# Kernel optimization log

Measured on AMD Instinct MI355X. Metric: run time of the kernel, lower is better.

The kernel has to match this reference:

```python
import jax, jax.numpy as jnp
import numpy as np
from math import pi as PI, log

B, N, D, K = 16, 16384, 64, 64


def setup_inputs() -> dict:
    key = jax.random.key(0)
    k1, k2, k3, k4 = jax.random.split(key, 4)
    x = jax.random.normal(k1, (B, N, D), dtype=jnp.float32)
    pi_w = jax.nn.softmax(jax.random.normal(k2, (K,), dtype=jnp.float32))  # mixture weights, sum to 1
    mu = jax.random.normal(k3, (K, D), dtype=jnp.float32)
    var = jax.random.uniform(k4, (K, D), dtype=jnp.float32, minval=0.5, maxval=1.5)  # diagonal variances
    return {"x": x, "pi": pi_w, "mu": mu, "var": var}


def reference(x, pi, mu, var):
    b, n, d = x.shape
    # --- gmm.predict_proba: diagonal-covariance Gaussian log-likelihoods + log pi, softmax over K ---
    inv_var = 1.0 / var                                   # (K, D)
    x2 = x * x                                            # (B, N, D)
    # Mahalanobis distance expanded via matmuls to avoid a (B,N,K,D) intermediate
    maha = (jnp.einsum('bnd,kd->bnk', x2, inv_var)
            - 2.0 * jnp.einsum('bnd,kd->bnk', x, mu * inv_var)
            + jnp.sum(mu * mu * inv_var, axis=-1))        # (B, N, K)
    log_det = jnp.sum(jnp.log(var), axis=-1)              # (K,)
    log_prob = -0.5 * (d * log(2.0 * PI) + log_det + maha)
    Q = jax.nn.softmax(log_prob + jnp.log(pi), axis=-1)   # (B, N, K) responsibilities
    # --- weighted reductions over N ---
    Q_sum = jnp.sum(Q, axis=1) / n                         # (B, K)
    Q_x = jnp.einsum('bnk,bnd->bkd', Q, x) / n             # (B, K, D)
    Q_x2 = jnp.einsum('bnk,bnd->bkd', Q, x2) / n           # (B, K, D)
    # --- Fisher-vector statistics ---
    d_pi = Q_sum - pi                                      # (B, K)
    qs = Q_sum[..., None]                                  # (B, K, 1)
    d_mu = Q_x - qs * mu
    d_sigma = -Q_x2 - qs * (mu * mu) + qs * var + 2.0 * Q_x * mu
    return jnp.concatenate([d_pi.reshape(b, -1), d_mu.reshape(b, -1), d_sigma.reshape(b, -1)], axis=1)
```

## Files before the change

kernel.cpp:

```cpp
#include <hip/hip_runtime.h>
#include <hip/hip_bf16.h>
#include <math.h>

#define B_  16
#define N_  16384
#define D_  64
#define K_  64
#define OUT_PER_B (K_ + 2*K_*D_)
#define CHUNKS 32
#define NTILES (N_ / CHUNKS / 64)

#define PART_STRIDE (64*4 + 2*4096*2)

typedef float f32x4 __attribute__((ext_vector_type(4)));
typedef short short8 __attribute__((ext_vector_type(8)));

union U8 { short8 s8; unsigned int u[4]; };

__device__ __forceinline__ unsigned short f2bf(float f) {
    union { float f; unsigned int u; } v; v.f = f;
    unsigned int r = v.u + 0x7FFFu + ((v.u >> 16) & 1u);
    return (unsigned short)(r >> 16);
}

__device__ __forceinline__ unsigned int f2bf2(float lo, float hi) {
    __hip_bfloat162 h = __float22bfloat162_rn(make_float2(lo, hi));
    unsigned int u;
    __builtin_memcpy(&u, &h, 4);
    return u;
}

__device__ __forceinline__ float bf2f(unsigned short u) {
    unsigned int v = ((unsigned int)u) << 16;
    float f;
    __builtin_memcpy(&f, &v, 4);
    return f;
}

__global__ __launch_bounds__(256, 2) void fv_main(const float* __restrict__ x,
                                                  const float* __restrict__ pi,
                                                  const float* __restrict__ mu,
                                                  const float* __restrict__ var,
                                                  char* __restrict__ partials) {
    __shared__ __align__(16) unsigned short QtS[2][64 * 72];
    __shared__ float qsum_s[4][64];
    __shared__ float red[256];
    __shared__ float c0s[64];

    const int t    = threadIdx.x;
    const int w    = t >> 6;
    const int lane = t & 63;
    const int r16  = lane & 15;
    const int q    = lane >> 4;

    {
        int k = t >> 2, pr = t & 3;
        float s = 0.0f;
        #pragma unroll
        for (int j = 0; j < 16; ++j) {
            int d = pr * 16 + j;
            float v = var[k * 64 + d];
            float m = mu[k * 64 + d];
            s += __logf(v) + m * m / v;
        }
        red[t] = s;
    }

    short8 wfrag[4][4];
    #pragma unroll
    for (int kt = 0; kt < 4; ++kt) {
        const int k = 16 * kt + r16;
        const float* vr = var + k * 64 + 8 * q;
        const float* mr = mu  + k * 64 + 8 * q;
        float vv[16], mm[16];
        *(float4*)&vv[0]  = *(const float4*)(vr);
        *(float4*)&vv[4]  = *(const float4*)(vr + 4);
        *(float4*)&vv[8]  = *(const float4*)(vr + 32);
        *(float4*)&vv[12] = *(const float4*)(vr + 36);
        *(float4*)&mm[0]  = *(const float4*)(mr);
        *(float4*)&mm[4]  = *(const float4*)(mr + 4);
        *(float4*)&mm[8]  = *(const float4*)(mr + 32);
        *(float4*)&mm[12] = *(const float4*)(mr + 36);
        float iv[16];
        #pragma unroll
        for (int i = 0; i < 16; ++i) iv[i] = 1.0f / vv[i];
        U8 h0, h1, h2, h3;
        #pragma unroll
        for (int i = 0; i < 4; ++i) {
            h0.u[i] = f2bf2(-0.5f * iv[2*i],     -0.5f * iv[2*i + 1]);
            h1.u[i] = f2bf2(-0.5f * iv[8 + 2*i], -0.5f * iv[8 + 2*i + 1]);
            h2.u[i] = f2bf2(mm[2*i] * iv[2*i],   mm[2*i+1] * iv[2*i + 1]);
            h3.u[i] = f2bf2(mm[8+2*i] * iv[8+2*i], mm[8+2*i+1] * iv[8+2*i+1]);
        }
        wfrag[kt][0] = h0.s8; wfrag[kt][1] = h1.s8;
        wfrag[kt][2] = h2.s8; wfrag[kt][3] = h3.s8;
    }

    __syncthreads();
    if ((t & 3) == 0) {
        int k = t >> 2;
        float sum = red[4 * k] + red[4 * k + 1] + red[4 * k + 2] + red[4 * k + 3];
        c0s[k] = __logf(pi[k]) - 0.5f * (117.6241322502f + sum);
    }
    __syncthreads();

    f32x4 c0v[4];
    #pragma unroll
    for (int kt = 0; kt < 4; ++kt)
        c0v[kt] = *(const f32x4*)&c0s[16 * kt + 4 * q];

    const int bi    = blockIdx.y;
    const int chunk = blockIdx.x;
    const int ppb   = N_ / CHUNKS;
    const float* xb = x + ((size_t)bi * N_ + (size_t)chunk * ppb) * D_;

    f32x4 accX[4]  = {};
    f32x4 accX2[4] = {};
    float qsacc[4][4] = {};

    const int rowoff = (16 * w + r16) * D_ + 8 * q;
    const int dcol   = 16 * w + r16;

    float4 va, vb, vc, vd;
    {
        const float* xr = xb + rowoff;
        va = *(const float4*)(xr);
        vb = *(const float4*)(xr + 4);
        vc = *(const float4*)(xr + 32);
        vd = *(const float4*)(xr + 36);
    }

    #pragma unroll 2
    for (int tile = 0; tile < NTILES; ++tile) {
        const float* xt = xb + (size_t)tile * 64 * D_;

        float vle[16];
        {
            const float* xc = xt + dcol;
            #pragma unroll
            for (int c = 0; c < 2; ++c)
                #pragma unroll
                for (int j = 0; j < 8; ++j)
                    vle[8 * c + j] = xc[(32 * c + 8 * q + j) * D_];
        }

        float4 nva, nvb, nvc, nvd;
        if (tile + 1 < NTILES) {
            const float* xr = xt + 64 * D_ + rowoff;
            nva = *(const float4*)(xr);
            nvb = *(const float4*)(xr + 4);
            nvc = *(const float4*)(xr + 32);
            nvd = *(const float4*)(xr + 36);
        }

        U8 fxa, fxb, fx2a, fx2b;
        fxa.u[0]  = f2bf2(va.x, va.y);           fxa.u[1]  = f2bf2(va.z, va.w);
        fxa.u[2]  = f2bf2(vb.x, vb.y);           fxa.u[3]  = f2bf2(vb.z, vb.w);
        fxb.u[0]  = f2bf2(vc.x, vc.y);           fxb.u[1]  = f2bf2(vc.z, vc.w);
        fxb.u[2]  = f2bf2(vd.x, vd.y);           fxb.u[3]  = f2bf2(vd.z, vd.w);
        fx2a.u[0] = f2bf2(va.x*va.x, va.y*va.y); fx2a.u[1] = f2bf2(va.z*va.z, va.w*va.w);
        fx2a.u[2] = f2bf2(vb.x*vb.x, vb.y*vb.y); fx2a.u[3] = f2bf2(vb.z*vb.z, vb.w*vb.w);
        fx2b.u[0] = f2bf2(vc.x*vc.x, vc.y*vc.y); fx2b.u[1] = f2bf2(vc.z*vc.z, vc.w*vc.w);
        fx2b.u[2] = f2bf2(vd.x*vd.x, vd.y*vd.y); fx2b.u[3] = f2bf2(vd.z*vd.z, vd.w*vd.w);

        float sc[4][4];
        #pragma unroll
        for (int kt = 0; kt < 4; ++kt) {
            f32x4 a = c0v[kt];
            a = __builtin_amdgcn_mfma_f32_16x16x32_bf16(wfrag[kt][0], fx2a.s8, a, 0, 0, 0);
            a = __builtin_amdgcn_mfma_f32_16x16x32_bf16(wfrag[kt][1], fx2b.s8, a, 0, 0, 0);
            a = __builtin_amdgcn_mfma_f32_16x16x32_bf16(wfrag[kt][2], fxa.s8,  a, 0, 0, 0);
            a = __builtin_amdgcn_mfma_f32_16x16x32_bf16(wfrag[kt][3], fxb.s8,  a, 0, 0, 0);
            sc[kt][0] = a[0]; sc[kt][1] = a[1]; sc[kt][2] = a[2]; sc[kt][3] = a[3];
        }

        float mx = sc[0][0];
        #pragma unroll
        for (int kt = 0; kt < 4; ++kt)
            #pragma unroll
            for (int rr = 0; rr < 4; ++rr) mx = fmaxf(mx, sc[kt][rr]);
        mx = fmaxf(mx, __shfl_xor(mx, 16));
        mx = fmaxf(mx, __shfl_xor(mx, 32));
        float z = 0.0f;
        #pragma unroll
        for (int kt = 0; kt < 4; ++kt)
            #pragma unroll
            for (int rr = 0; rr < 4; ++rr) {
                sc[kt][rr] = __expf(sc[kt][rr] - mx);
                z += sc[kt][rr];
            }
        z += __shfl_xor(z, 16);
        z += __shfl_xor(z, 32);
        float inv = 1.0f / z;
        const int p = 16 * w + r16;
        unsigned short* Qb = QtS[tile & 1];
        #pragma unroll
        for (int kt = 0; kt < 4; ++kt) {
            #pragma unroll
            for (int rr = 0; rr < 4; rr += 2) {
                float q0 = sc[kt][rr] * inv;
                float q1 = sc[kt][rr + 1] * inv;
                qsacc[kt][rr]     += q0;
                qsacc[kt][rr + 1] += q1;
                unsigned int pk = f2bf2(q0, q1);
                Qb[(16 * kt + 4 * q + rr)     * 72 + p] = (unsigned short)pk;
                Qb[(16 * kt + 4 * q + rr + 1) * 72 + p] = (unsigned short)(pk >> 16);
            }
        }

        asm volatile("s_waitcnt lgkmcnt(0)\n\ts_barrier" ::: "memory");

        U8 fxp0, fxp1, fx2p0, fx2p1;
        #pragma unroll
        for (int i = 0; i < 4; ++i) {
            float a0 = vle[2 * i], a1 = vle[2 * i + 1];
            float b0 = vle[8 + 2 * i], b1 = vle[8 + 2 * i + 1];
            fxp0.u[i]  = f2bf2(a0, a1);
            fxp1.u[i]  = f2bf2(b0, b1);
            fx2p0.u[i] = f2bf2(a0 * a0, a1 * a1);
            fx2p1.u[i] = f2bf2(b0 * b0, b1 * b1);
        }
        #pragma unroll
        for (int kt = 0; kt < 4; ++kt) {
            const unsigned short* qr = &Qb[(16 * kt + r16) * 72 + 8 * q];
            short8 aq0 = *(const short8*)(const void*)(qr);
            short8 aq1 = *(const short8*)(const void*)(qr + 32);
            accX[kt]  = __builtin_amdgcn_mfma_f32_16x16x32_bf16(aq0, fxp0.s8,  accX[kt],  0, 0, 0);
            accX2[kt] = __builtin_amdgcn_mfma_f32_16x16x32_bf16(aq0, fx2p0.s8, accX2[kt], 0, 0, 0);
            accX[kt]  = __builtin_amdgcn_mfma_f32_16x16x32_bf16(aq1, fxp1.s8,  accX[kt],  0, 0, 0);
            accX2[kt] = __builtin_amdgcn_mfma_f32_16x16x32_bf16(aq1, fx2p1.s8, accX2[kt], 0, 0, 0);
        }

        va = nva; vb = nvb; vc = nvc; vd = nvd;
    }

    char* rec = partials + ((size_t)bi * CHUNKS + chunk) * PART_STRIDE;
    float* part_qs = (float*)rec;
    unsigned short* part_qx  = (unsigned short*)(rec + 256);
    unsigned short* part_qx2 = part_qx + 4096;
    #pragma unroll
    for (int kt = 0; kt < 4; ++kt)
        #pragma unroll
        for (int rr = 0; rr < 4; ++rr) {
            int k = 16 * kt + 4 * q + rr;
            part_qx [k * 64 + 16 * w + r16] = f2bf(accX[kt][rr]);
            part_qx2[k * 64 + 16 * w + r16] = f2bf(accX2[kt][rr]);
        }
    #pragma unroll
    for (int kt = 0; kt < 4; ++kt)
        #pragma unroll
        for (int rr = 0; rr < 4; ++rr) {
            float v = qsacc[kt][rr];
            v += __shfl_xor(v, 1);
            v += __shfl_xor(v, 2);
            v += __shfl_xor(v, 4);
            v += __shfl_xor(v, 8);
            if (r16 == 0) qsum_s[w][16 * kt + 4 * q + rr] = v;
        }
    __syncthreads();
    if (t < 64)
        part_qs[t] = qsum_s[0][t] + qsum_s[1][t] + qsum_s[2][t] + qsum_s[3][t];
}

__global__ __launch_bounds__(256) void fv_finalize(const float* __restrict__ pi,
                                                   const float* __restrict__ mu,
                                                   const float* __restrict__ var,
                                                   const char* __restrict__ partials,
                                                   float* __restrict__ out) {
    int g = blockIdx.x * 256 + threadIdx.x;
    if (g >= B_ * OUT_PER_B) return;
    int b   = g / OUT_PER_B;
    int pos = g - b * OUT_PER_B;
    const char* base = partials + (size_t)b * CHUNKS * PART_STRIDE;
    const float invN = 1.0f / (float)N_;

    if (pos < 64) {
        float qs = 0.0f;
        for (int c = 0; c < CHUNKS; ++c)
            qs += ((const float*)(base + c * PART_STRIDE))[pos];
        out[g] = qs * invN - pi[pos];
    } else if (pos < 64 + 4096) {
        int idx = pos - 64;
        int k = idx >> 6;
        float qs = 0.0f, qx = 0.0f;
        for (int c = 0; c < CHUNKS; ++c) {
            const char* r = base + c * PART_STRIDE;
            qs += ((const float*)r)[k];
            qx += bf2f(((const unsigned short*)(r + 256))[idx]);
        }
        out[g] = (qx - qs * mu[idx]) * invN;
    } else {
        int idx = pos - 64 - 4096;
        int k = idx >> 6;
        float qs = 0.0f, qx = 0.0f, qx2 = 0.0f;
        for (int c = 0; c < CHUNKS; ++c) {
            const char* r = base + c * PART_STRIDE;
            qs  += ((const float*)r)[k];
            qx  += bf2f(((const unsigned short*)(r + 256))[idx]);
            qx2 += bf2f(((const unsigned short*)(r + 256))[4096 + idx]);
        }
        float m = mu[idx], v = var[idx];
        out[g] = (-qx2 - qs * m * m + qs * v + 2.0f * qx * m) * invN;
    }
}

extern "C" void kernel_launch(void* const* d_in, const int* in_sizes, int n_in,
                              void* d_out, int out_size, void* d_ws, size_t ws_size,
                              hipStream_t stream) {
    const float* x   = (const float*)d_in[0];
    const float* pi  = (const float*)d_in[1];
    const float* mu  = (const float*)d_in[2];
    const float* var = (const float*)d_in[3];
    char* partials = (char*)d_ws;

    fv_main<<<dim3(CHUNKS, B_), 256, 0, stream>>>(x, pi, mu, var, partials);
    int total = B_ * OUT_PER_B;
    fv_finalize<<<(total + 255) / 256, 256, 0, stream>>>(pi, mu, var, partials,
                                                         (float*)d_out);
}
```

Measured before the change: 120.1 us.

## Double chunk count, raise occupancy, restructure finalize per (batch, component)

Doubles the number of N-chunks per batch so the main kernel launches 1024 blocks instead of 512, and raises the launch-bounds min-blocks hint from 2 to 4 to allow more resident waves. The finalize kernel is rewritten so each block handles one (b,k) pair. Four thread groups split the chunk reduction and combine through shared memory, and Q_sum, Q_x and Q_x2 are computed together. This aims to expose more parallelism on the GPU. The cost is twice the partials traffic, and register pressure under the tighter launch bound could cause spills.

```diff
diff --git a/kernel.cpp b/kernel.cpp
--- a/kernel.cpp
+++ b/kernel.cpp
@@ -7,7 +7,7 @@
 #define D_  64
 #define K_  64
 #define OUT_PER_B (K_ + 2*K_*D_)
-#define CHUNKS 32
+#define CHUNKS 64
 #define NTILES (N_ / CHUNKS / 64)
 
 #define PART_STRIDE (64*4 + 2*4096*2)
@@ -37,7 +37,7 @@
     return f;
 }
 
-__global__ __launch_bounds__(256, 2) void fv_main(const float* __restrict__ x,
+__global__ __launch_bounds__(256, 4) void fv_main(const float* __restrict__ x,
                                                   const float* __restrict__ pi,
                                                   const float* __restrict__ mu,
                                                   const float* __restrict__ var,
@@ -267,40 +267,42 @@
                                                    const float* __restrict__ var,
                                                    const char* __restrict__ partials,
                                                    float* __restrict__ out) {
-    int g = blockIdx.x * 256 + threadIdx.x;
-    if (g >= B_ * OUT_PER_B) return;
-    int b   = g / OUT_PER_B;
-    int pos = g - b * OUT_PER_B;
+    const int bk = blockIdx.x;
+    const int b  = bk >> 6;
+    const int k  = bk & 63;
+    const int t  = threadIdx.x;
+    const int d  = t & 63;
+    const int cg = t >> 6;
+
     const char* base = partials + (size_t)b * CHUNKS * PART_STRIDE;
-    const float invN = 1.0f / (float)N_;
-
-    if (pos < 64) {
-        float qs = 0.0f;
-        for (int c = 0; c < CHUNKS; ++c)
-            qs += ((const float*)(base + c * PART_STRIDE))[pos];
-        out[g] = qs * invN - pi[pos];
-    } else if (pos < 64 + 4096) {
-        int idx = pos - 64;
-        int k = idx >> 6;
-        float qs = 0.0f, qx = 0.0f;
-        for (int c = 0; c < CHUNKS; ++c) {
-            const char* r = base + c * PART_STRIDE;
-            qs += ((const float*)r)[k];
-            qx += bf2f(((const unsigned short*)(r + 256))[idx]);
-        }
-        out[g] = (qx - qs * mu[idx]) * invN;
-    } else {
-        int idx = pos - 64 - 4096;
-        int k = idx >> 6;
-        float qs = 0.0f, qx = 0.0f, qx2 = 0.0f;
-        for (int c = 0; c < CHUNKS; ++c) {
-            const char* r = base + c * PART_STRIDE;
-            qs  += ((const float*)r)[k];
-            qx  += bf2f(((const unsigned short*)(r + 256))[idx]);
-            qx2 += bf2f(((const unsigned short*)(r + 256))[4096 + idx]);
-        }
-        float m = mu[idx], v = var[idx];
-        out[g] = (-qx2 - qs * m * m + qs * v + 2.0f * qx * m) * invN;
+
+    float qs = 0.0f, qx = 0.0f, qx2 = 0.0f;
+    for (int c = cg; c < CHUNKS; c += 4) {
+        const char* r = base + (size_t)c * PART_STRIDE;
+        qs  += ((const float*)r)[k];
+        qx  += bf2f(((const unsigned short*)(r + 256))[k * 64 + d]);
+        qx2 += bf2f(((const unsigned short*)(r + 256))[4096 + k * 64 + d]);
+    }
+
+    __shared__ float sQx[4][64];
+    __shared__ float sQx2[4][64];
+    __shared__ float sQs[4];
+    sQx[cg][d]  = qx;
+    sQx2[cg][d] = qx2;
+    if (d == 0) sQs[cg] = qs;
+    __syncthreads();
+
+    if (cg == 0) {
+        const float invN = 1.0f / (float)N_;
+        float QX  = sQx[0][d]  + sQx[1][d]  + sQx[2][d]  + sQx[3][d];
+        float QX2 = sQx2[0][d] + sQx2[1][d] + sQx2[2][d] + sQx2[3][d];
+        float QS  = sQs[0] + sQs[1] + sQs[2] + sQs[3];
+        float m = mu[k * 64 + d];
+        float v = var[k * 64 + d];
+        float* ob = out + (size_t)b * OUT_PER_B;
+        if (d == 0) ob[k] = QS * invN - pi[k];
+        ob[64 + k * 64 + d]        = (QX - QS * m) * invN;
+        ob[64 + 4096 + k * 64 + d] = (-QX2 - QS * m * m + QS * v + 2.0f * QX * m) * invN;
     }
 }
 
@@ -314,7 +316,5 @@
     char* partials = (char*)d_ws;
 
     fv_main<<<dim3(CHUNKS, B_), 256, 0, stream>>>(x, pi, mu, var, partials);
-    int total = B_ * OUT_PER_B;
-    fv_finalize<<<(total + 255) / 256, 256, 0, stream>>>(pi, mu, var, partials,
-                                                         (float*)d_out);
-}
+    fv_finalize<<<B_ * K_, 256, 0, stream>>>(pi, mu, var, partials, (float*)d_out);
+}
```

Result: slower. 267.6 us (+122.9%).
